# Kernel tuning notes

Measured on AMD Instinct MI355X. Metric: run time of the kernel, lower is better.

## Reference

```python
import math
import jax, jax.numpy as jnp
import numpy as np

B, S, D = 8, 1024, 1024
H, DK = 16, 64
NUM_BUCKETS, MAX_DIST = 32, 128


def _relative_position_bucket(relative_position, num_buckets=NUM_BUCKETS, max_distance=MAX_DIST):
    # bidirectional (encoder, is_decoder=False)
    num_buckets //= 2  # 16
    rb = (relative_position > 0).astype(jnp.int32) * num_buckets
    rp = jnp.abs(relative_position)
    max_exact = num_buckets // 2  # 8
    is_small = rp < max_exact
    rp_safe = jnp.maximum(rp, 1)  # avoid log(0); masked out by is_small anyway
    large = max_exact + (
        jnp.log(rp_safe.astype(jnp.float32) / max_exact)
        / math.log(max_distance / max_exact)
        * (num_buckets - max_exact)
    ).astype(jnp.int32)
    large = jnp.minimum(large, num_buckets - 1)
    return rb + jnp.where(is_small, rp, large)


def compute_bias(rel_bias, q_len, k_len):
    ctx = jnp.arange(q_len, dtype=jnp.int32)[:, None]
    mem = jnp.arange(k_len, dtype=jnp.int32)[None, :]
    buckets = _relative_position_bucket(mem - ctx)  # [q_len, k_len]
    vals = rel_bias[buckets]  # [q_len, k_len, H]
    return jnp.transpose(vals, (2, 0, 1))[None]  # [1, H, q_len, k_len]


def setup_inputs() -> dict:
    key = jax.random.key(0)
    ks = jax.random.split(key, 6)
    sd = 1.0 / math.sqrt(D)
    return {
        "hidden_states": jax.random.normal(ks[0], (B, S, D), jnp.float32),
        "wq": jax.random.normal(ks[1], (D, H * DK), jnp.float32) * sd,
        "wk": jax.random.normal(ks[2], (D, H * DK), jnp.float32) * sd,
        "wv": jax.random.normal(ks[3], (D, H * DK), jnp.float32) * sd,
        "wo": jax.random.normal(ks[4], (H * DK, D), jnp.float32) * sd,
        "rel_bias": jax.random.normal(ks[5], (NUM_BUCKETS, H), jnp.float32),
    }


def reference(hidden_states, wq, wk, wv, wo, rel_bias):
    b, s, _ = hidden_states.shape

    def shape_heads(x):  # [b, s, H*DK] -> [b, H, s, DK]
        return jnp.transpose(x.reshape(b, s, H, DK), (0, 2, 1, 3))

    q = shape_heads(hidden_states @ wq)
    k = shape_heads(hidden_states @ wk)
    v = shape_heads(hidden_states @ wv)

    # T5 attention: NO 1/sqrt(dk) scaling
    scores = jnp.einsum("bhqd,bhkd->bhqk", q, k)
    bias = compute_bias(rel_bias, s, s)  # [1, H, s, s]
    attn = jax.nn.softmax(scores + bias, axis=-1)

    ctx = jnp.einsum("bhqk,bhkd->bhqd", attn, v)  # [b, H, s, DK]
    ctx = jnp.transpose(ctx, (0, 2, 1, 3)).reshape(b, s, H * DK)
    return ctx @ wo  # [b, s, D]
```

## Files before the change

### kernel.cpp

```cpp
#include <hip/hip_runtime.h>
#include <stdint.h>

typedef __attribute__((ext_vector_type(8))) short bf16x8;
typedef __attribute__((ext_vector_type(4))) float f32x4;
typedef __attribute__((ext_vector_type(16))) float f32x16;
typedef __attribute__((ext_vector_type(8))) unsigned short ushort8;
typedef __attribute__((ext_vector_type(4))) unsigned short ushort4v;

#define MFMA16(a, b, c) __builtin_amdgcn_mfma_f32_16x16x32_bf16((a), (b), (c), 0, 0, 0)
#define MFMA32(a, b, c) __builtin_amdgcn_mfma_f32_32x32x16_bf16((a), (b), (c), 0, 0, 0)

#define SLEN 1024
#define NHEAD 16
#define HDIM 64
#define DMODEL 1024
#define NROWS 8192
#define LOG2E 1.44269504088896340736f

__device__ __forceinline__ unsigned short f2bf(float f) {
  unsigned int u = __float_as_uint(f);
  u += 0x7FFFu + ((u >> 16) & 1u);
  return (unsigned short)(u >> 16);
}

__device__ __forceinline__ float fast_exp2(float x) {
#if __has_builtin(__builtin_amdgcn_exp2f)
  return __builtin_amdgcn_exp2f(x);
#else
  float r; asm("v_exp_f32 %0, %1" : "=v"(r) : "v"(x)); return r;
#endif
}

__device__ __forceinline__ unsigned int cvt_pk_bf16(float lo, float hi) {
  unsigned int r;
  asm("v_cvt_pk_bf16_f32 %0, %1, %2" : "=v"(r) : "v"(lo), "v"(hi));
  return r;
}

__device__ __forceinline__ void gload_lds16(const void* g, void* l) {
  __builtin_amdgcn_global_load_lds(
      (const __attribute__((address_space(1))) void*)g,
      (__attribute__((address_space(3))) void*)l, 16, 0, 0);
}

__global__ __launch_bounds__(256) void k_convert_x(const float* __restrict__ x,
                                                   unsigned short* __restrict__ xb, int n) {
  int i = blockIdx.x * 256 + threadIdx.x;
  int idx = i * 8;
  if (idx >= n) return;
  float4 a = *(const float4*)(x + idx);
  float4 b = *(const float4*)(x + idx + 4);
  ushort8 o;
  o[0] = f2bf(a.x); o[1] = f2bf(a.y); o[2] = f2bf(a.z); o[3] = f2bf(a.w);
  o[4] = f2bf(b.x); o[5] = f2bf(b.y); o[6] = f2bf(b.z); o[7] = f2bf(b.w);
  *(ushort8*)(xb + idx) = o;
}

__global__ __launch_bounds__(256) void k_transpose_w(
    const float* __restrict__ w0, const float* __restrict__ w1,
    const float* __restrict__ w2, const float* __restrict__ w3,
    unsigned short* __restrict__ o0, unsigned short* __restrict__ o1,
    unsigned short* __restrict__ o2, unsigned short* __restrict__ o3) {
  int z = blockIdx.z;
  const float* w = (z == 0) ? w0 : (z == 1) ? w1 : (z == 2) ? w2 : w3;
  unsigned short* o = (z == 0) ? o0 : (z == 1) ? o1 : (z == 2) ? o2 : o3;
  __shared__ unsigned short tile[32][33];
  int bx = blockIdx.x & 31, by = blockIdx.x >> 5;
  int tid = threadIdx.x;
#pragma unroll
  for (int p = 0; p < 4; ++p) {
    int idx = tid + p * 256;
    int r = idx >> 5, c = idx & 31;
    tile[r][c] = f2bf(w[(size_t)(by * 32 + r) * DMODEL + bx * 32 + c]);
  }
  __syncthreads();
#pragma unroll
  for (int p = 0; p < 4; ++p) {
    int idx = tid + p * 256;
    int r = idx >> 5, c = idx & 31;
    o[(size_t)(bx * 32 + r) * DMODEL + by * 32 + c] = tile[c][r];
  }
}

__global__ __launch_bounds__(256) void k_bias_table(const float* __restrict__ rel_bias,
                                                    float* __restrict__ bt) {
  int i = blockIdx.x * 256 + threadIdx.x;
  if (i >= NHEAD * 2047) return;
  int h = i / 2047, rdx = i % 2047;
  int rel = rdx - 1023;
  int rb = (rel > 0) ? 16 : 0;
  int rp = (rel < 0) ? -rel : rel;
  int bucket;
  if (rp < 8) {
    bucket = rb + rp;
  } else {
    int large;
    if (rp >= 91) {
      large = 15;
    } else {
      int nb = 31 - __clz(rp);
      long long sq = (long long)rp * rp;
      int f2 = 2 * nb + ((sq >= (1LL << (2 * nb + 1))) ? 1 : 0);
      large = 8 + (f2 - 6);
      if (large > 15) large = 15;
    }
    bucket = rb + large;
  }
  bt[h * 2048 + rdx] = rel_bias[bucket * 16 + h] * LOG2E;
}

__device__ __forceinline__ void gemm_tile_lds(const unsigned short* __restrict__ A,
                                              const unsigned short* __restrict__ Bt,
                                              int K, int tm, int tn,
                                              unsigned short* As, unsigned short* Bs,
                                              f32x4 acc[4][4]) {
  const int tid = threadIdx.x;
  const int lane = tid & 63;
  const int w = tid >> 6;
  const int wr = w >> 1, wc = w & 1;
  const int g = lane >> 4, t = lane & 15;
  const int NKT = K >> 6;

  auto stageT = [&](int bufo, int ko) {
#pragma unroll
    for (int j = 0; j < 4; ++j) {
      const int r = w * 32 + j * 8 + (lane >> 3);
      const int lc = (lane & 7) ^ (r & 7);
      gload_lds16(A + (size_t)(tm + r) * K + ko + lc * 8, As + bufo + (w * 4 + j) * 512);
      gload_lds16(Bt + (size_t)(tn + r) * K + ko + lc * 8, Bs + bufo + (w * 4 + j) * 512);
    }
  };

  f32x4 z = {0.f, 0.f, 0.f, 0.f};
#pragma unroll
  for (int mi = 0; mi < 4; ++mi)
#pragma unroll
    for (int ni = 0; ni < 4; ++ni) acc[mi][ni] = z;

  stageT(0, 0);
  __syncthreads();

#pragma unroll 1
  for (int kt = 0; kt < NKT; ++kt) {
    const int cur = (kt & 1) * 8192;
    if (kt + 1 < NKT) stageT(cur ^ 8192, (kt + 1) * 64);

    bf16x8 af[2][4], bfr[2][4];
#pragma unroll
    for (int kk = 0; kk < 2; ++kk)
#pragma unroll
      for (int mi = 0; mi < 4; ++mi) {
        const int ra = wr * 64 + mi * 16 + t;
        const int pa = ((kk << 2) | g) ^ (ra & 7);
        af[kk][mi] = *(const bf16x8*)&As[cur + ra * 64 + pa * 8];
      }
#pragma unroll
    for (int kk = 0; kk < 2; ++kk)
#pragma unroll
      for (int ni = 0; ni < 4; ++ni) {
        const int rb = wc * 64 + ni * 16 + t;
        const int pb = ((kk << 2) | g) ^ (rb & 7);
        bfr[kk][ni] = *(const bf16x8*)&Bs[cur + rb * 64 + pb * 8];
      }
#pragma unroll
    for (int kk = 0; kk < 2; ++kk)
#pragma unroll
      for (int mi = 0; mi < 4; ++mi)
#pragma unroll
        for (int ni = 0; ni < 4; ++ni)
          acc[mi][ni] = MFMA16(af[kk][mi], bfr[kk][ni], acc[mi][ni]);

    __syncthreads();
  }
}

__global__ __launch_bounds__(256) void k_gemm_qkv(
    const unsigned short* __restrict__ Xb,
    const unsigned short* __restrict__ Wqt, const unsigned short* __restrict__ Wkt,
    const unsigned short* __restrict__ Wvt,
    unsigned short* __restrict__ Qb, unsigned short* __restrict__ Kb,
    unsigned short* __restrict__ Vt) {
  __shared__ alignas(16) unsigned short As[2 * 128 * 64];
  __shared__ alignas(16) unsigned short Bs[2 * 128 * 64];
  int z = blockIdx.z;
  const unsigned short* Bt = (z == 0) ? Wqt : (z == 1) ? Wkt : Wvt;
  const int wid = (blockIdx.x & 7) * 64 + (blockIdx.x >> 3);
  int tm = (wid >> 3) * 128, tn = (wid & 7) * 128;
  f32x4 acc[4][4];
  gemm_tile_lds(Xb, Bt, DMODEL, tm, tn, As, Bs, acc);

  const int lane = threadIdx.x & 63, w = threadIdx.x >> 6;
  const int wr = w >> 1, wc = w & 1, g = lane >> 4, t = lane & 15;
  if (z < 2) {
    unsigned short* O = (z == 0) ? Qb : Kb;
#pragma unroll
    for (int mi = 0; mi < 4; ++mi)
#pragma unroll
      for (int ni = 0; ni < 4; ++ni)
#pragma unroll
        for (int r = 0; r < 4; ++r) {
          int m = tm + wr * 64 + mi * 16 + g * 4 + r;
          int n = tn + wc * 64 + ni * 16 + t;
          int b = m >> 10, s = m & 1023, h = n >> 6, d = n & 63;
          O[((size_t)((b * 16 + h) * 1024 + s)) * 64 + d] = f2bf(acc[mi][ni][r]);
        }
  } else {
#pragma unroll
    for (int mi = 0; mi < 4; ++mi)
#pragma unroll
      for (int ni = 0; ni < 4; ++ni) {
        int m0 = tm + wr * 64 + mi * 16 + g * 4;
        int n = tn + wc * 64 + ni * 16 + t;
        int b = m0 >> 10, s0 = m0 & 1023, h = n >> 6, d = n & 63;
        ushort4v pk;
#pragma unroll
        for (int r = 0; r < 4; ++r) pk[r] = f2bf(acc[mi][ni][r]);
        *(ushort4v*)&Vt[((size_t)((b * 16 + h) * 64 + d) * 1024) + s0] = pk;
      }
  }
}

__global__ __launch_bounds__(512) void k_attn(
    const unsigned short* __restrict__ Qb, const unsigned short* __restrict__ Kb,
    const unsigned short* __restrict__ Vt, const float* __restrict__ bt,
    unsigned short* __restrict__ ctx) {
  __shared__ alignas(16) unsigned short Ks[2][64 * 64];
  __shared__ alignas(16) unsigned short Vs[2][64 * 64];
  __shared__ alignas(16) float Lb[376];
  __shared__ float sred[8][32];

  const int wid = ((blockIdx.x & 7) << 6) | (blockIdx.x >> 3);
  const int bh = wid >> 2, qb = wid & 3;
  const int h = bh & 15, b = bh >> 4;
  const int tid = threadIdx.x;
  const int lane = tid & 63, w = tid >> 6;
  const int ql = lane & 31, hi = lane >> 5;
  const int q0 = qb * 256 + w * 32;
  const int q = q0 + ql;

  for (int i = tid; i < 376; i += 512) Lb[i] = bt[(size_t)h * 2048 + 837 + i];

  const unsigned short* Qp = Qb + (size_t)bh * SLEN * 64;
  const unsigned short* Kp = Kb + (size_t)bh * SLEN * 64;
  const unsigned short* Vp = Vt + (size_t)bh * 64 * SLEN;

  bf16x8 bq[4];
#pragma unroll
  for (int c = 0; c < 4; ++c)
    bq[c] = *(const bf16x8*)(Qp + (size_t)q * 64 + c * 16 + hi * 8);

  const f32x16 z16 = {0.f,0.f,0.f,0.f,0.f,0.f,0.f,0.f,0.f,0.f,0.f,0.f,0.f,0.f,0.f,0.f};
  f32x16 o0 = z16, o1 = z16;
  float m = -INFINITY, l = 0.f;

  auto stage = [&](int buf, int kbase) {
    int lb = w * 1024 + lane * 16;
    int row = lb >> 7;
    int lc = ((lb >> 4) & 7) ^ (row & 7);
    gload_lds16(Kp + (size_t)(kbase + row) * 64 + lc * 8, &Ks[buf][w * 512]);
    gload_lds16(Vp + (size_t)row * SLEN + kbase + lc * 8, &Vs[buf][w * 512]);
  };

  stage(0, 0);
  __syncthreads();
  const float cpos = Lb[186 + 91], cneg = Lb[186 - 91];

  int cur = 0;
#pragma unroll 1
  for (int kt = 0; kt < 16; ++kt) {
    const int kbase = kt * 64;
    if (kt != 15) stage(cur ^ 1, kbase + 64);

    const char* Kc = (const char*)Ks[cur];
    const char* Vc = (const char*)Vs[cur];

#pragma unroll
    for (int hh = 0; hh < 2; ++hh) {
      const int kb32 = kbase + hh * 32;

      bf16x8 ak[4];
#pragma unroll
      for (int c = 0; c < 4; ++c) {
        const int ph = ((c << 1) | hi) ^ (ql & 7);
        ak[c] = *(const bf16x8*)(Kc + (hh * 32 + ql) * 128 + ph * 16);
      }

      bf16x8 bv00, bv01, bv10, bv11;
      {
        const int p0 = ((hh << 2) | hi) ^ (ql & 7);
        const int p1 = ((hh << 2) | 2 | hi) ^ (ql & 7);
        bv00 = *(const bf16x8*)(Vc + ql * 128 + p0 * 16);
        bv01 = *(const bf16x8*)(Vc + (32 + ql) * 128 + p0 * 16);
        bv10 = *(const bf16x8*)(Vc + ql * 128 + p1 * 16);
        bv11 = *(const bf16x8*)(Vc + (32 + ql) * 128 + p1 * 16);
      }

      f32x16 s = z16;
      __builtin_amdgcn_s_setprio(1);
#pragma unroll
      for (int c = 0; c < 4; ++c) s = MFMA32(ak[c], bq[c], s);
      __builtin_amdgcn_s_setprio(0);

      const bool farp = (kb32 >= q0 + 122);
      const bool farn = (kb32 + 122 <= q0);
      if (farp || farn) {
        const float c = farp ? cpos : cneg;
#pragma unroll
        for (int r = 0; r < 16; ++r) s[r] = fmaf(s[r], LOG2E, c);
      } else {
        const int base = kb32 - q + 186 + hi * 4;
#pragma unroll
        for (int r = 0; r < 16; ++r)
          s[r] = fmaf(s[r], LOG2E, Lb[base + (r & 3) + 8 * (r >> 2)]);
      }

      float vm = s[0];
#pragma unroll
      for (int r = 1; r < 16; ++r) vm = fmaxf(vm, s[r]);
      vm = fmaxf(vm, __shfl_xor(vm, 32));

      if (__any(vm > m + 8.0f)) {
        const float mn = fmaxf(m, vm);
        const float sc = fast_exp2(m - mn);
        m = mn;
        l *= sc;
        sred[w][ql] = sc;
        __builtin_amdgcn_wave_barrier();
#pragma unroll
        for (int r = 0; r < 16; ++r) {
          const float sr = sred[w][(r & 3) + 8 * (r >> 2) + hi * 4];
          o0[r] *= sr; o1[r] *= sr;
        }
        __builtin_amdgcn_wave_barrier();
      }

      float p[16];
      float ls = 0.f;
#pragma unroll
      for (int r = 0; r < 16; ++r) { p[r] = fast_exp2(s[r] - m); ls += p[r]; }
      l += ls + __shfl_xor(ls, 32);

      unsigned int wv[8], xv[8];
#pragma unroll
      for (int i = 0; i < 8; ++i) wv[i] = cvt_pk_bf16(p[2 * i], p[2 * i + 1]);
#pragma unroll
      for (int i = 0; i < 8; ++i) xv[i] = __shfl_xor(wv[i], 32);
      union { unsigned int u[4]; bf16x8 v; } pa0, pa1;
      pa0.u[0] = hi ? xv[2] : wv[0];
      pa0.u[1] = hi ? xv[3] : wv[1];
      pa0.u[2] = hi ? wv[2] : xv[0];
      pa0.u[3] = hi ? wv[3] : xv[1];
      pa1.u[0] = hi ? xv[6] : wv[4];
      pa1.u[1] = hi ? xv[7] : wv[5];
      pa1.u[2] = hi ? wv[6] : xv[4];
      pa1.u[3] = hi ? wv[7] : xv[5];

      __builtin_amdgcn_s_setprio(1);
      o0 = MFMA32(pa0.v, bv00, o0);
      o0 = MFMA32(pa1.v, bv10, o0);
      o1 = MFMA32(pa0.v, bv01, o1);
      o1 = MFMA32(pa1.v, bv11, o1);
      __builtin_amdgcn_s_setprio(0);
    }

    __syncthreads();
    cur ^= 1;
  }

  const float inv = 1.0f / l;
  sred[w][ql] = inv;
  __builtin_amdgcn_wave_barrier();
#pragma unroll
  for (int r = 0; r < 16; ++r) {
    const float ir = sred[w][(r & 3) + 8 * (r >> 2) + hi * 4];
    const int qq = q0 + (r & 3) + 8 * (r >> 2) + hi * 4;
    const size_t base = ((size_t)(b * 1024 + qq)) * 1024 + h * 64 + ql;
    ctx[base] = f2bf(o0[r] * ir);
    ctx[base + 32] = f2bf(o1[r] * ir);
  }
}

__global__ __launch_bounds__(256) void k_gemm_out(
    const unsigned short* __restrict__ Cb, const unsigned short* __restrict__ Wot,
    float* __restrict__ out) {
  __shared__ alignas(16) unsigned short As[2 * 128 * 64];
  __shared__ alignas(16) unsigned short Bs[2 * 128 * 64];
  const int wid = (blockIdx.x & 7) * 64 + (blockIdx.x >> 3);
  int tm = (wid >> 3) * 128, tn = (wid & 7) * 128;
  f32x4 acc[4][4];
  gemm_tile_lds(Cb, Wot, DMODEL, tm, tn, As, Bs, acc);

  const int lane = threadIdx.x & 63, w = threadIdx.x >> 6;
  const int wr = w >> 1, wc = w & 1, g = lane >> 4, t = lane & 15;
#pragma unroll
  for (int mi = 0; mi < 4; ++mi)
#pragma unroll
    for (int ni = 0; ni < 4; ++ni)
#pragma unroll
      for (int r = 0; r < 4; ++r) {
        int m = tm + wr * 64 + mi * 16 + g * 4 + r;
        int n = tn + wc * 64 + ni * 16 + t;
        out[(size_t)m * DMODEL + n] = acc[mi][ni][r];
      }
}

extern "C" void kernel_launch(void* const* d_in, const int* in_sizes, int n_in,
                              void* d_out, int out_size, void* d_ws, size_t ws_size,
                              hipStream_t stream) {
  const float* hs = (const float*)d_in[0];
  const float* wq = (const float*)d_in[1];
  const float* wk = (const float*)d_in[2];
  const float* wv = (const float*)d_in[3];
  const float* wo = (const float*)d_in[4];
  const float* rb = (const float*)d_in[5];

  char* ws = (char*)d_ws;
  unsigned short* Xb  = (unsigned short*)(ws + 0);
  unsigned short* Wqt = (unsigned short*)(ws + 16777216);
  unsigned short* Wkt = (unsigned short*)(ws + 18874368);
  unsigned short* Wvt = (unsigned short*)(ws + 20971520);
  unsigned short* Wot = (unsigned short*)(ws + 23068672);
  unsigned short* Qb  = (unsigned short*)(ws + 25165824);
  unsigned short* Kb  = (unsigned short*)(ws + 41943040);
  unsigned short* Vt  = (unsigned short*)(ws + 58720256);
  unsigned short* Cb  = (unsigned short*)(ws + 75497472);
  float* bt           = (float*)(ws + 92274688);

  k_convert_x<<<4096, 256, 0, stream>>>(hs, Xb, NROWS * DMODEL);
  k_transpose_w<<<dim3(1024, 1, 4), 256, 0, stream>>>(wq, wk, wv, wo, Wqt, Wkt, Wvt, Wot);
  k_bias_table<<<128, 256, 0, stream>>>(rb, bt);
  k_gemm_qkv<<<dim3(512, 1, 3), 256, 0, stream>>>(Xb, Wqt, Wkt, Wvt, Qb, Kb, Vt);
  k_attn<<<512, 512, 0, stream>>>(Qb, Kb, Vt, bt, Cb);
  k_gemm_out<<<512, 256, 0, stream>>>(Cb, Wot, (float*)d_out);
}
```

Measured before the change: 171.4 us.

## Process two 32-query groups per wave in attention to reuse K/V fragments

The attention kernel now launches 256 threads per block instead of 512, and each wave handles 64 queries as two 32-row groups. The K and V fragments read from shared memory are reused across both groups, which halves LDS reads per unit of work. Each thread now issues two global-to-LDS loads per stage. The cost is roughly double the accumulator and softmax-state registers per wave and fewer waves per block, which may lower occupancy and reduce latency hiding.

```diff
diff --git a/kernel.cpp b/kernel.cpp
--- a/kernel.cpp
+++ b/kernel.cpp
@@ -220,14 +220,14 @@
   }
 }
 
-__global__ __launch_bounds__(512) void k_attn(
+__global__ __launch_bounds__(256) void k_attn(
     const unsigned short* __restrict__ Qb, const unsigned short* __restrict__ Kb,
     const unsigned short* __restrict__ Vt, const float* __restrict__ bt,
     unsigned short* __restrict__ ctx) {
   __shared__ alignas(16) unsigned short Ks[2][64 * 64];
   __shared__ alignas(16) unsigned short Vs[2][64 * 64];
   __shared__ alignas(16) float Lb[376];
-  __shared__ float sred[8][32];
+  __shared__ float sred[4][32];
 
   const int wid = ((blockIdx.x & 7) << 6) | (blockIdx.x >> 3);
   const int bh = wid >> 2, qb = wid & 3;
@@ -235,30 +235,35 @@
   const int tid = threadIdx.x;
   const int lane = tid & 63, w = tid >> 6;
   const int ql = lane & 31, hi = lane >> 5;
-  const int q0 = qb * 256 + w * 32;
-  const int q = q0 + ql;
-
-  for (int i = tid; i < 376; i += 512) Lb[i] = bt[(size_t)h * 2048 + 837 + i];
+  const int q0 = qb * 256 + w * 64;
+
+  for (int i = tid; i < 376; i += 256) Lb[i] = bt[(size_t)h * 2048 + 837 + i];
 
   const unsigned short* Qp = Qb + (size_t)bh * SLEN * 64;
   const unsigned short* Kp = Kb + (size_t)bh * SLEN * 64;
   const unsigned short* Vp = Vt + (size_t)bh * 64 * SLEN;
 
-  bf16x8 bq[4];
-#pragma unroll
-  for (int c = 0; c < 4; ++c)
-    bq[c] = *(const bf16x8*)(Qp + (size_t)q * 64 + c * 16 + hi * 8);
+  bf16x8 bq[2][4];
+#pragma unroll
+  for (int G = 0; G < 2; ++G)
+#pragma unroll
+    for (int c = 0; c < 4; ++c)
+      bq[G][c] = *(const bf16x8*)(Qp + (size_t)(q0 + G * 32 + ql) * 64 + c * 16 + hi * 8);
 
   const f32x16 z16 = {0.f,0.f,0.f,0.f,0.f,0.f,0.f,0.f,0.f,0.f,0.f,0.f,0.f,0.f,0.f,0.f};
-  f32x16 o0 = z16, o1 = z16;
-  float m = -INFINITY, l = 0.f;
+  f32x16 o[2][2];
+  o[0][0] = z16; o[0][1] = z16; o[1][0] = z16; o[1][1] = z16;
+  float m[2] = {-INFINITY, -INFINITY}, l[2] = {0.f, 0.f};
 
   auto stage = [&](int buf, int kbase) {
-    int lb = w * 1024 + lane * 16;
-    int row = lb >> 7;
-    int lc = ((lb >> 4) & 7) ^ (row & 7);
-    gload_lds16(Kp + (size_t)(kbase + row) * 64 + lc * 8, &Ks[buf][w * 512]);
-    gload_lds16(Vp + (size_t)row * SLEN + kbase + lc * 8, &Vs[buf][w * 512]);
+#pragma unroll
+    for (int j = 0; j < 2; ++j) {
+      int lb = w * 2048 + j * 1024 + lane * 16;
+      int row = lb >> 7;
+      int lc = ((lb >> 4) & 7) ^ (row & 7);
+      gload_lds16(Kp + (size_t)(kbase + row) * 64 + lc * 8, &Ks[buf][w * 1024 + j * 512]);
+      gload_lds16(Vp + (size_t)row * SLEN + kbase + lc * 8, &Vs[buf][w * 1024 + j * 512]);
+    }
   };
 
   stage(0, 0);
@@ -295,88 +300,98 @@
         bv11 = *(const bf16x8*)(Vc + (32 + ql) * 128 + p1 * 16);
       }
 
-      f32x16 s = z16;
-      __builtin_amdgcn_s_setprio(1);
-#pragma unroll
-      for (int c = 0; c < 4; ++c) s = MFMA32(ak[c], bq[c], s);
-      __builtin_amdgcn_s_setprio(0);
-
-      const bool farp = (kb32 >= q0 + 122);
-      const bool farn = (kb32 + 122 <= q0);
-      if (farp || farn) {
-        const float c = farp ? cpos : cneg;
-#pragma unroll
-        for (int r = 0; r < 16; ++r) s[r] = fmaf(s[r], LOG2E, c);
-      } else {
-        const int base = kb32 - q + 186 + hi * 4;
-#pragma unroll
-        for (int r = 0; r < 16; ++r)
-          s[r] = fmaf(s[r], LOG2E, Lb[base + (r & 3) + 8 * (r >> 2)]);
-      }
-
-      float vm = s[0];
-#pragma unroll
-      for (int r = 1; r < 16; ++r) vm = fmaxf(vm, s[r]);
-      vm = fmaxf(vm, __shfl_xor(vm, 32));
-
-      if (__any(vm > m + 8.0f)) {
-        const float mn = fmaxf(m, vm);
-        const float sc = fast_exp2(m - mn);
-        m = mn;
-        l *= sc;
-        sred[w][ql] = sc;
-        __builtin_amdgcn_wave_barrier();
-#pragma unroll
-        for (int r = 0; r < 16; ++r) {
-          const float sr = sred[w][(r & 3) + 8 * (r >> 2) + hi * 4];
-          o0[r] *= sr; o1[r] *= sr;
+#pragma unroll
+      for (int G = 0; G < 2; ++G) {
+        const int q0G = q0 + G * 32;
+        const int qG = q0G + ql;
+
+        f32x16 s = z16;
+        __builtin_amdgcn_s_setprio(1);
+#pragma unroll
+        for (int c = 0; c < 4; ++c) s = MFMA32(ak[c], bq[G][c], s);
+        __builtin_amdgcn_s_setprio(0);
+
+        const bool farp = (kb32 >= q0G + 122);
+        const bool farn = (kb32 + 122 <= q0G);
+        if (farp || farn) {
+          const float c = farp ? cpos : cneg;
+#pragma unroll
+          for (int r = 0; r < 16; ++r) s[r] = fmaf(s[r], LOG2E, c);
+        } else {
+          const int base = kb32 - qG + 186 + hi * 4;
+#pragma unroll
+          for (int r = 0; r < 16; ++r)
+            s[r] = fmaf(s[r], LOG2E, Lb[base + (r & 3) + 8 * (r >> 2)]);
         }
-        __builtin_amdgcn_wave_barrier();
-      }
-
-      float p[16];
-      float ls = 0.f;
-#pragma unroll
-      for (int r = 0; r < 16; ++r) { p[r] = fast_exp2(s[r] - m); ls += p[r]; }
-      l += ls + __shfl_xor(ls, 32);
-
-      unsigned int wv[8], xv[8];
-#pragma unroll
-      for (int i = 0; i < 8; ++i) wv[i] = cvt_pk_bf16(p[2 * i], p[2 * i + 1]);
-#pragma unroll
-      for (int i = 0; i < 8; ++i) xv[i] = __shfl_xor(wv[i], 32);
-      union { unsigned int u[4]; bf16x8 v; } pa0, pa1;
-      pa0.u[0] = hi ? xv[2] : wv[0];
-      pa0.u[1] = hi ? xv[3] : wv[1];
-      pa0.u[2] = hi ? wv[2] : xv[0];
-      pa0.u[3] = hi ? wv[3] : xv[1];
-      pa1.u[0] = hi ? xv[6] : wv[4];
-      pa1.u[1] = hi ? xv[7] : wv[5];
-      pa1.u[2] = hi ? wv[6] : xv[4];
-      pa1.u[3] = hi ? wv[7] : xv[5];
-
-      __builtin_amdgcn_s_setprio(1);
-      o0 = MFMA32(pa0.v, bv00, o0);
-      o0 = MFMA32(pa1.v, bv10, o0);
-      o1 = MFMA32(pa0.v, bv01, o1);
-      o1 = MFMA32(pa1.v, bv11, o1);
-      __builtin_amdgcn_s_setprio(0);
+
+        float vm = s[0];
+#pragma unroll
+        for (int r = 1; r < 16; ++r) vm = fmaxf(vm, s[r]);
+        vm = fmaxf(vm, __shfl_xor(vm, 32));
+
+        if (__any(vm > m[G] + 8.0f)) {
+          const float mn = fmaxf(m[G], vm);
+          const float sc = fast_exp2(m[G] - mn);
+          m[G] = mn;
+          l[G] *= sc;
+          sred[w][ql] = sc;
+          __builtin_amdgcn_wave_barrier();
+#pragma unroll
+          for (int r = 0; r < 16; ++r) {
+            const float sr = sred[w][(r & 3) + 8 * (r >> 2) + hi * 4];
+            o[G][0][r] *= sr; o[G][1][r] *= sr;
+          }
+          __builtin_amdgcn_wave_barrier();
+        }
+
+        float p[16];
+        float ls = 0.f;
+#pragma unroll
+        for (int r = 0; r < 16; ++r) { p[r] = fast_exp2(s[r] - m[G]); ls += p[r]; }
+        l[G] += ls + __shfl_xor(ls, 32);
+
+        unsigned int wv[8], xv[8];
+#pragma unroll
+        for (int i = 0; i < 8; ++i) wv[i] = cvt_pk_bf16(p[2 * i], p[2 * i + 1]);
+#pragma unroll
+        for (int i = 0; i < 8; ++i) xv[i] = __shfl_xor(wv[i], 32);
+        union { unsigned int u[4]; bf16x8 v; } pa0, pa1;
+        pa0.u[0] = hi ? xv[2] : wv[0];
+        pa0.u[1] = hi ? xv[3] : wv[1];
+        pa0.u[2] = hi ? wv[2] : xv[0];
+        pa0.u[3] = hi ? wv[3] : xv[1];
+        pa1.u[0] = hi ? xv[6] : wv[4];
+        pa1.u[1] = hi ? xv[7] : wv[5];
+        pa1.u[2] = hi ? wv[6] : xv[4];
+        pa1.u[3] = hi ? wv[7] : xv[5];
+
+        __builtin_amdgcn_s_setprio(1);
+        o[G][0] = MFMA32(pa0.v, bv00, o[G][0]);
+        o[G][0] = MFMA32(pa1.v, bv10, o[G][0]);
+        o[G][1] = MFMA32(pa0.v, bv01, o[G][1]);
+        o[G][1] = MFMA32(pa1.v, bv11, o[G][1]);
+        __builtin_amdgcn_s_setprio(0);
+      }
     }
 
     __syncthreads();
     cur ^= 1;
   }
 
-  const float inv = 1.0f / l;
-  sred[w][ql] = inv;
-  __builtin_amdgcn_wave_barrier();
-#pragma unroll
-  for (int r = 0; r < 16; ++r) {
-    const float ir = sred[w][(r & 3) + 8 * (r >> 2) + hi * 4];
-    const int qq = q0 + (r & 3) + 8 * (r >> 2) + hi * 4;
-    const size_t base = ((size_t)(b * 1024 + qq)) * 1024 + h * 64 + ql;
-    ctx[base] = f2bf(o0[r] * ir);
-    ctx[base + 32] = f2bf(o1[r] * ir);
+#pragma unroll
+  for (int G = 0; G < 2; ++G) {
+    const float inv = 1.0f / l[G];
+    __builtin_amdgcn_wave_barrier();
+    sred[w][ql] = inv;
+    __builtin_amdgcn_wave_barrier();
+#pragma unroll
+    for (int r = 0; r < 16; ++r) {
+      const float ir = sred[w][(r & 3) + 8 * (r >> 2) + hi * 4];
+      const int qq = q0 + G * 32 + (r & 3) + 8 * (r >> 2) + hi * 4;
+      const size_t base = ((size_t)(b * 1024 + qq)) * 1024 + h * 64 + ql;
+      ctx[base] = f2bf(o[G][0][r] * ir);
+      ctx[base + 32] = f2bf(o[G][1][r] * ir);
+    }
   }
 }
 
@@ -430,6 +445,6 @@
   k_transpose_w<<<dim3(1024, 1, 4), 256, 0, stream>>>(wq, wk, wv, wo, Wqt, Wkt, Wvt, Wot);
   k_bias_table<<<128, 256, 0, stream>>>(rb, bt);
   k_gemm_qkv<<<dim3(512, 1, 3), 256, 0, stream>>>(Xb, Wqt, Wkt, Wvt, Qb, Kb, Vt);
-  k_attn<<<512, 512, 0, stream>>>(Qb, Kb, Vt, bt, Cb);
+  k_attn<<<512, 256, 0, stream>>>(Qb, Kb, Vt, bt, Cb);
   k_gemm_out<<<512, 256, 0, stream>>>(Cb, Wot, (float*)d_out);
 }
```

Result: slower. 202.3 us (+18.1%).
